# Performance work log

Measured on AMD Instinct MI355X. Metric: run time of the kernel, lower is better.

The kernel has to match this reference:

```python
import jax, jax.numpy as jnp
import numpy as np

DIM = 1024
N_HEADS = 16
HEAD_DIM = DIM // N_HEADS
SCALE = HEAD_DIM ** -0.5


def setup_inputs() -> dict:
    key = jax.random.key(0)
    ks = jax.random.split(key, 5)
    B, N = 2, 2048
    x = jax.random.normal(ks[0], (B, N, DIM), dtype=jnp.float32)
    # torch Linear: y = x @ W.T + b, W shape (out, in)
    qkv_w = jax.random.normal(ks[1], (3 * DIM, DIM), dtype=jnp.float32) * (DIM ** -0.5)
    qkv_b = jax.random.normal(ks[2], (3 * DIM,), dtype=jnp.float32) * 0.02
    proj_w = jax.random.normal(ks[3], (DIM, DIM), dtype=jnp.float32) * (DIM ** -0.5)
    proj_b = jax.random.normal(ks[4], (DIM,), dtype=jnp.float32) * 0.02
    return {"x": x, "qkv_w": qkv_w, "qkv_b": qkv_b, "proj_w": proj_w, "proj_b": proj_b}


def reference(x, qkv_w, qkv_b, proj_w, proj_b):
    B, N, D = x.shape
    qkv = x @ qkv_w.T + qkv_b                      # [B, N, 3D]
    qkv = qkv.reshape(B, N, 3, N_HEADS, HEAD_DIM)
    qkv = jnp.transpose(qkv, (2, 0, 3, 1, 4))      # [3, B, H, N, hd]
    q, k, v = qkv[0], qkv[1], qkv[2]
    dp = jnp.einsum('bhqd,bhkd->bhqk', q, k) * SCALE  # [B, H, N, N]
    attn = jax.nn.softmax(dp, axis=-1)
    wa = jnp.einsum('bhqk,bhkd->bhqd', attn, v)    # [B, H, N, hd]
    wa = jnp.transpose(wa, (0, 2, 1, 3)).reshape(B, N, D)
    return wa @ proj_w.T + proj_b
```

## Files before the change

### kernel.cpp

```cpp
#include <hip/hip_runtime.h>

#define BATCH 2
#define SEQ   2048
#define DIM   1024
#define NHEAD 16
#define HD    64
#define BH    (BATCH * NHEAD)
#define SCALE 0.125f
#define LOG2E 1.44269504f
#define NTK   16

typedef __attribute__((ext_vector_type(8))) short short8;
typedef __attribute__((ext_vector_type(4))) float f32x4;
typedef __attribute__((ext_vector_type(16))) float f32x16;
typedef __attribute__((ext_vector_type(2))) unsigned int uint2v;

#define MFMA16(a, b, c) __builtin_amdgcn_mfma_f32_16x16x32_bf16(a, b, c, 0, 0, 0)
#define MFMA32(a, b, c) __builtin_amdgcn_mfma_f32_32x32x16_bf16(a, b, c, 0, 0, 0)

__device__ __forceinline__ ushort f2bf(float f) {
    union { float f; unsigned u; } v;
    v.f = f;
    unsigned r = (v.u + 0x7FFF + ((v.u >> 16) & 1)) >> 16;
    return (ushort)r;
}

__device__ __forceinline__ uint4 ld8f_bf16(const float* p) {
    float4 f0 = *(const float4*)p;
    float4 f1 = *(const float4*)(p + 4);
    union { ushort us[8]; uint4 v; } u;
    u.us[0] = f2bf(f0.x); u.us[1] = f2bf(f0.y);
    u.us[2] = f2bf(f0.z); u.us[3] = f2bf(f0.w);
    u.us[4] = f2bf(f1.x); u.us[5] = f2bf(f1.y);
    u.us[6] = f2bf(f1.z); u.us[7] = f2bf(f1.w);
    return u.v;
}

__device__ __forceinline__ void gl_lds16(const ushort* g, ushort* l) {
    __builtin_amdgcn_global_load_lds(
        (const __attribute__((address_space(1))) unsigned int*)g,
        (__attribute__((address_space(3))) unsigned int*)l,
        16, 0, 0);
}

#define N_X  (BATCH * SEQ * DIM)
#define N_QW (3 * DIM * DIM)
#define N_PW (DIM * DIM)

__global__ __launch_bounds__(256) void cvt_kernel(
    const float* __restrict__ x, const float* __restrict__ qw,
    const float* __restrict__ pw, ushort* __restrict__ xb,
    ushort* __restrict__ qwb, ushort* __restrict__ pwb)
{
    const int i = (blockIdx.x * 256 + threadIdx.x) * 8;
    if (i < N_X)  *(uint4*)(xb  + i) = ld8f_bf16(x  + i);
    if (i < N_QW) *(uint4*)(qwb + i) = ld8f_bf16(qw + i);
    if (i < N_PW) *(uint4*)(pwb + i) = ld8f_bf16(pw + i);
}

template <int MODE, int WM, typename TOUT>
__global__ __launch_bounds__(256, 2) void gemm_bt(
    const ushort* __restrict__ A, const ushort* __restrict__ W,
    const float* __restrict__ bias, TOUT* __restrict__ out,
    int M, int Nout, int K)
{
    constexpr int BM = 2 * WM * 16;
    __shared__ __align__(16) ushort As[2][BM * 32];
    __shared__ __align__(16) ushort Bs[2][128 * 32];

    const int tid  = threadIdx.x;
    const int wave = tid >> 6, lane = tid & 63;
    const int quad = lane >> 4, l16 = lane & 15;
    const int wm = wave >> 1, wn = wave & 1;
    const int m0 = blockIdx.y * BM, n0 = blockIdx.x * 128;

    const int c0 = tid, c1 = tid + 256;
    const ushort* gA0 = A + (size_t)(m0 + (c0 >> 2)) * K + (c0 & 3) * 8;
    const ushort* gA1 = A + (size_t)(m0 + (c1 >> 2)) * K + (c1 & 3) * 8;
    const ushort* gB0 = W + (size_t)(n0 + (c0 >> 2)) * K + (c0 & 3) * 8;
    const ushort* gB1 = W + (size_t)(n0 + (c1 >> 2)) * K + (c1 & 3) * 8;

#define STAGE_G(buf, k0)                                                  \
    {                                                                     \
        gl_lds16(gA0 + (k0), &As[buf][(wave * 64) * 8]);                  \
        if (WM == 4) gl_lds16(gA1 + (k0), &As[buf][(wave * 64 + 256) * 8]); \
        gl_lds16(gB0 + (k0), &Bs[buf][(wave * 64) * 8]);                  \
        gl_lds16(gB1 + (k0), &Bs[buf][(wave * 64 + 256) * 8]);            \
    }

    f32x4 acc[WM][4];
#pragma unroll
    for (int i = 0; i < WM; i++)
#pragma unroll
        for (int j = 0; j < 4; j++) acc[i][j] = (f32x4){0.f, 0.f, 0.f, 0.f};

    const int KT = K >> 5;
    STAGE_G(0, 0)

    for (int kt = 0; kt < KT; kt++) {
        const int cur = kt & 1;
        __syncthreads();
        if (kt + 1 < KT) STAGE_G(cur ^ 1, (kt + 1) * 32)

        short8 af[WM], bfr[4];
#pragma unroll
        for (int mt = 0; mt < WM; mt++)
            af[mt] = *(const short8*)&As[cur][(wm * (WM * 16) + mt * 16 + l16) * 32 + quad * 8];
#pragma unroll
        for (int nt = 0; nt < 4; nt++)
            bfr[nt] = *(const short8*)&Bs[cur][(wn * 64 + nt * 16 + l16) * 32 + quad * 8];
#pragma unroll
        for (int mt = 0; mt < WM; mt++)
#pragma unroll
            for (int nt = 0; nt < 4; nt++)
                acc[mt][nt] = MFMA16(af[mt], bfr[nt], acc[mt][nt]);
    }

#pragma unroll
    for (int nt = 0; nt < 4; nt++) {
        const int n = n0 + wn * 64 + nt * 16 + l16;
        const float bv = bias[n];
#pragma unroll
        for (int mt = 0; mt < WM; mt++) {
            const int mBase = m0 + wm * (WM * 16) + mt * 16 + quad * 4;
#pragma unroll
            for (int r = 0; r < 4; r++) {
                const int m = mBase + r;
                float v = acc[mt][nt][r] + bv;
                if (MODE == 0) {
                    const int which = n >> 10, rem = n & 1023;
                    const int h = rem >> 6, d = rem & 63;
                    const int b = m >> 11, nq = m & 2047;
                    const int bh = b * NHEAD + h;
                    if (which == 0) v *= (SCALE * LOG2E);
                    size_t idx;
                    if (which == 2)
                        idx = (size_t)2 * BH * SEQ * HD + ((size_t)bh * HD + d) * SEQ + nq;
                    else
                        idx = (size_t)which * BH * SEQ * HD + ((size_t)bh * SEQ + nq) * HD + d;
                    ((ushort*)out)[idx] = f2bf(v);
                } else {
                    ((float*)out)[(size_t)m * Nout + n] = v;
                }
            }
        }
    }
#undef STAGE_G
}

__global__ __launch_bounds__(512, 4) void attn_kernel(
    const ushort* __restrict__ qkv, ushort* __restrict__ wa)
{
    __shared__ __align__(16) ushort Ks[2][2][64 * 64];
    __shared__ __align__(16) ushort Vs[2][2][64 * 64];

    const int tid  = threadIdx.x;
    const int wave = tid >> 6, lane = tid & 63;
    const int l31  = lane & 31, hb = lane >> 5;
    const int h2 = wave >> 2, w4 = wave & 3;

    const int l = blockIdx.x;
    const int bh = (l & 7) + 8 * (l >> 7);
    const int qi = (l >> 3) & 15;
    const int b = bh >> 4, head = bh & 15;

    const size_t hOff = (size_t)bh * SEQ * HD;
    const ushort* Q  = qkv + hOff;
    const ushort* Kg = qkv + (size_t)BH * SEQ * HD + hOff;
    const ushort* Vt = qkv + (size_t)2 * BH * SEQ * HD + hOff;
    const int q0 = qi * 128 + w4 * 32;

    short8 qf[4];
#pragma unroll
    for (int i = 0; i < 4; i++)
        qf[i] = *(const short8*)&Q[(size_t)(q0 + l31) * HD + i * 16 + hb * 8];

    f32x16 o0, o1;
#pragma unroll
    for (int r = 0; r < 16; r++) { o0[r] = 0.f; o1[r] = 0.f; }
    f32x4 lacc = (f32x4){0.f, 0.f, 0.f, 0.f};

    const int rr = lane >> 3;
    const int cc = ((lane & 7) ^ rr) * 8;
    const ushort* KgL = Kg + rr * HD + cc;
    const ushort* VtL = Vt + (size_t)rr * SEQ + cc;

#define STAGE(buf, kt)                                                          \
    {                                                                           \
        const size_t kO = (size_t)h2 * 1024 + (size_t)(kt) * 64;                \
        gl_lds16(KgL + (kO + w4 * 16    ) * HD, &Ks[h2][buf][(w4 * 16    ) * 64]); \
        gl_lds16(KgL + (kO + w4 * 16 + 8) * HD, &Ks[h2][buf][(w4 * 16 + 8) * 64]); \
        gl_lds16(VtL + (size_t)(w4 * 16    ) * SEQ + kO, &Vs[h2][buf][(w4 * 16    ) * 64]); \
        gl_lds16(VtL + (size_t)(w4 * 16 + 8) * SEQ + kO, &Vs[h2][buf][(w4 * 16 + 8) * 64]); \
    }

    STAGE(0, 0)

    const int swz = l31 & 7;

    for (int kt = 0; kt < NTK; kt++) {
        const int cur = kt & 1;
        __syncthreads();
        if (kt + 1 < NTK) STAGE(cur ^ 1, kt + 1)

        const ushort* kb_ = &Ks[h2][cur][0];
        const ushort* vb_ = &Vs[h2][cur][0];

        f32x16 z0, z1;
#pragma unroll
        for (int r = 0; r < 16; r++) { z0[r] = 0.f; z1[r] = 0.f; }

        __builtin_amdgcn_s_setprio(1);
#pragma unroll
        for (int i = 0; i < 4; i++) {
            short8 ka0 = *(const short8*)&kb_[(l31     ) * 64 + (((2*i + hb) ^ swz) * 8)];
            short8 ka1 = *(const short8*)&kb_[(32 + l31) * 64 + (((2*i + hb) ^ swz) * 8)];
            z0 = MFMA32(ka0, qf[i], z0);
            z1 = MFMA32(ka1, qf[i], z1);
        }
        __builtin_amdgcn_s_setprio(0);

        unsigned u[2][8];
#pragma unroll
        for (int r = 0; r < 16; r++) {
            const float p0 = __builtin_amdgcn_exp2f(z0[r]);
            const float p1 = __builtin_amdgcn_exp2f(z1[r]);
            z0[r] = p0; z1[r] = p1;
            lacc[r & 3] += p0 + p1;
        }
#pragma unroll
        for (int m = 0; m < 8; m++) {
            unsigned pk;
            asm("v_cvt_pk_bf16_f32 %0, %1, %2"
                : "=v"(pk) : "v"(z0[2*m]), "v"(z0[2*m + 1]));
            u[0][m] = pk;
            asm("v_cvt_pk_bf16_f32 %0, %1, %2"
                : "=v"(pk) : "v"(z1[2*m]), "v"(z1[2*m + 1]));
            u[1][m] = pk;
        }

        __builtin_amdgcn_s_setprio(1);
#pragma unroll
        for (int i = 0; i < 4; i++) {
            const int kb = i >> 1, ii = i & 1;
            uint2v s0 = __builtin_amdgcn_permlane32_swap(
                u[kb][4*ii + 0], u[kb][4*ii + 2], false, false);
            uint2v s1 = __builtin_amdgcn_permlane32_swap(
                u[kb][4*ii + 1], u[kb][4*ii + 3], false, false);
            union { unsigned w[4]; short8 s; } pf;
            pf.w[0] = s0[0]; pf.w[1] = s1[0]; pf.w[2] = s0[1]; pf.w[3] = s1[1];
            short8 vb0 = *(const short8*)&vb_[(l31     ) * 64 + (((2*i + hb) ^ swz) * 8)];
            short8 vb1 = *(const short8*)&vb_[(32 + l31) * 64 + (((2*i + hb) ^ swz) * 8)];
            o0 = MFMA32(pf.s, vb0, o0);
            o1 = MFMA32(pf.s, vb1, o1);
        }
        __builtin_amdgcn_s_setprio(0);
    }

    __syncthreads();

    float* Osc = (float*)&Ks[0][0][0];
    float* Lsc = (float*)&Vs[0][0][0];

    float lsum = lacc[0] + lacc[1] + lacc[2] + lacc[3];
    lsum += __shfl_xor(lsum, 32);
    if (lane < 32) Lsc[wave * 32 + l31] = lsum;

    if (h2 == 1) {
#pragma unroll
        for (int r = 0; r < 16; r++) {
            const int qr = (r & 3) + 8 * (r >> 2) + 4 * hb;
            Osc[w4 * 2048 + qr * 64 + l31]      = o0[r];
            Osc[w4 * 2048 + qr * 64 + 32 + l31] = o1[r];
        }
    }
    __syncthreads();

    if (h2 == 0) {
        const float inv = 1.f / (Lsc[w4 * 32 + l31] + Lsc[(4 + w4) * 32 + l31]);
#pragma unroll
        for (int r = 0; r < 16; r++) {
            const int qr = (r & 3) + 8 * (r >> 2) + 4 * hb;
            const float iv = __shfl(inv, qr);
            const float v0 = o0[r] + Osc[w4 * 2048 + qr * 64 + l31];
            const float v1 = o1[r] + Osc[w4 * 2048 + qr * 64 + 32 + l31];
            ushort* dst = wa + ((size_t)(b * SEQ + q0 + qr)) * DIM + head * HD + l31;
            dst[0]  = f2bf(v0 * iv);
            dst[32] = f2bf(v1 * iv);
        }
    }
#undef STAGE
}

extern "C" void kernel_launch(void* const* d_in, const int* in_sizes, int n_in,
                              void* d_out, int out_size, void* d_ws, size_t ws_size,
                              hipStream_t stream)
{
    const float* x      = (const float*)d_in[0];
    const float* qkv_w  = (const float*)d_in[1];
    const float* qkv_b  = (const float*)d_in[2];
    const float* proj_w = (const float*)d_in[3];
    const float* proj_b = (const float*)d_in[4];
    float* out = (float*)d_out;

    ushort* xb  = (ushort*)d_ws;
    ushort* qwb = xb  + (size_t)N_X;
    ushort* pwb = qwb + (size_t)N_QW;
    ushort* qkv = pwb + (size_t)N_PW;
    ushort* wa  = qkv + (size_t)3 * BH * SEQ * HD;

    const int M = BATCH * SEQ;
    dim3 blk(256);

    cvt_kernel<<<dim3((N_X / 8 + 255) / 256), blk, 0, stream>>>(
        x, qkv_w, proj_w, xb, qwb, pwb);

    gemm_bt<0, 4, ushort><<<dim3((3 * DIM) / 128, M / 128), blk, 0, stream>>>(
        xb, qwb, qkv_b, qkv, M, 3 * DIM, DIM);

    attn_kernel<<<dim3(512), dim3(512), 0, stream>>>(qkv, wa);

    gemm_bt<1, 2, float><<<dim3(DIM / 128, M / 64), blk, 0, stream>>>(
        wa, pwb, proj_b, out, M, DIM, DIM);
}
```

Baseline: 186.7 us.

## Give each attention wave 64 query rows to reuse K/V LDS fragments

```diff
diff --git a/kernel.cpp b/kernel.cpp
--- a/kernel.cpp
+++ b/kernel.cpp
@@ -148,7 +148,7 @@
 #undef STAGE_G
 }
 
-__global__ __launch_bounds__(512, 4) void attn_kernel(
+__global__ __launch_bounds__(256, 2) void attn_kernel(
     const ushort* __restrict__ qkv, ushort* __restrict__ wa)
 {
     __shared__ __align__(16) ushort Ks[2][2][64 * 64];
@@ -157,7 +157,7 @@
     const int tid  = threadIdx.x;
     const int wave = tid >> 6, lane = tid & 63;
     const int l31  = lane & 31, hb = lane >> 5;
-    const int h2 = wave >> 2, w4 = wave & 3;
+    const int h2 = wave >> 1, wq = wave & 1;
 
     const int l = blockIdx.x;
     const int bh = (l & 7) + 8 * (l >> 7);
@@ -168,17 +168,20 @@
     const ushort* Q  = qkv + hOff;
     const ushort* Kg = qkv + (size_t)BH * SEQ * HD + hOff;
     const ushort* Vt = qkv + (size_t)2 * BH * SEQ * HD + hOff;
-    const int q0 = qi * 128 + w4 * 32;
-
-    short8 qf[4];
-#pragma unroll
-    for (int i = 0; i < 4; i++)
-        qf[i] = *(const short8*)&Q[(size_t)(q0 + l31) * HD + i * 16 + hb * 8];
-
-    f32x16 o0, o1;
-#pragma unroll
-    for (int r = 0; r < 16; r++) { o0[r] = 0.f; o1[r] = 0.f; }
-    f32x4 lacc = (f32x4){0.f, 0.f, 0.f, 0.f};
+    const int q0 = qi * 128 + wq * 64;
+
+    short8 qf0[4], qf1[4];
+#pragma unroll
+    for (int i = 0; i < 4; i++) {
+        qf0[i] = *(const short8*)&Q[(size_t)(q0      + l31) * HD + i * 16 + hb * 8];
+        qf1[i] = *(const short8*)&Q[(size_t)(q0 + 32 + l31) * HD + i * 16 + hb * 8];
+    }
+
+    f32x16 o00, o01, o10, o11;
+#pragma unroll
+    for (int r = 0; r < 16; r++) { o00[r] = 0.f; o01[r] = 0.f; o10[r] = 0.f; o11[r] = 0.f; }
+    f32x4 lacc0 = (f32x4){0.f, 0.f, 0.f, 0.f};
+    f32x4 lacc1 = (f32x4){0.f, 0.f, 0.f, 0.f};
 
     const int rr = lane >> 3;
     const int cc = ((lane & 7) ^ rr) * 8;
@@ -188,10 +191,14 @@
 #define STAGE(buf, kt)                                                          \
     {                                                                           \
         const size_t kO = (size_t)h2 * 1024 + (size_t)(kt) * 64;                \
-        gl_lds16(KgL + (kO + w4 * 16    ) * HD, &Ks[h2][buf][(w4 * 16    ) * 64]); \
-        gl_lds16(KgL + (kO + w4 * 16 + 8) * HD, &Ks[h2][buf][(w4 * 16 + 8) * 64]); \
-        gl_lds16(VtL + (size_t)(w4 * 16    ) * SEQ + kO, &Vs[h2][buf][(w4 * 16    ) * 64]); \
-        gl_lds16(VtL + (size_t)(w4 * 16 + 8) * SEQ + kO, &Vs[h2][buf][(w4 * 16 + 8) * 64]); \
+        gl_lds16(KgL + (kO + wq * 32     ) * HD, &Ks[h2][buf][(wq * 32     ) * 64]); \
+        gl_lds16(KgL + (kO + wq * 32 +  8) * HD, &Ks[h2][buf][(wq * 32 +  8) * 64]); \
+        gl_lds16(KgL + (kO + wq * 32 + 16) * HD, &Ks[h2][buf][(wq * 32 + 16) * 64]); \
+        gl_lds16(KgL + (kO + wq * 32 + 24) * HD, &Ks[h2][buf][(wq * 32 + 24) * 64]); \
+        gl_lds16(VtL + (size_t)(wq * 32     ) * SEQ + kO, &Vs[h2][buf][(wq * 32     ) * 64]); \
+        gl_lds16(VtL + (size_t)(wq * 32 +  8) * SEQ + kO, &Vs[h2][buf][(wq * 32 +  8) * 64]); \
+        gl_lds16(VtL + (size_t)(wq * 32 + 16) * SEQ + kO, &Vs[h2][buf][(wq * 32 + 16) * 64]); \
+        gl_lds16(VtL + (size_t)(wq * 32 + 24) * SEQ + kO, &Vs[h2][buf][(wq * 32 + 24) * 64]); \
     }
 
     STAGE(0, 0)
@@ -206,37 +213,45 @@
         const ushort* kb_ = &Ks[h2][cur][0];
         const ushort* vb_ = &Vs[h2][cur][0];
 
-        f32x16 z0, z1;
-#pragma unroll
-        for (int r = 0; r < 16; r++) { z0[r] = 0.f; z1[r] = 0.f; }
+        f32x16 z00, z01, z10, z11;
+#pragma unroll
+        for (int r = 0; r < 16; r++) { z00[r] = 0.f; z01[r] = 0.f; z10[r] = 0.f; z11[r] = 0.f; }
 
         __builtin_amdgcn_s_setprio(1);
 #pragma unroll
         for (int i = 0; i < 4; i++) {
             short8 ka0 = *(const short8*)&kb_[(l31     ) * 64 + (((2*i + hb) ^ swz) * 8)];
             short8 ka1 = *(const short8*)&kb_[(32 + l31) * 64 + (((2*i + hb) ^ swz) * 8)];
-            z0 = MFMA32(ka0, qf[i], z0);
-            z1 = MFMA32(ka1, qf[i], z1);
+            z00 = MFMA32(ka0, qf0[i], z00);
+            z01 = MFMA32(ka1, qf0[i], z01);
+            z10 = MFMA32(ka0, qf1[i], z10);
+            z11 = MFMA32(ka1, qf1[i], z11);
         }
         __builtin_amdgcn_s_setprio(0);
 
-        unsigned u[2][8];
+        unsigned u0[2][8], u1[2][8];
 #pragma unroll
         for (int r = 0; r < 16; r++) {
-            const float p0 = __builtin_amdgcn_exp2f(z0[r]);
-            const float p1 = __builtin_amdgcn_exp2f(z1[r]);
-            z0[r] = p0; z1[r] = p1;
-            lacc[r & 3] += p0 + p1;
+            const float a0 = __builtin_amdgcn_exp2f(z00[r]);
+            const float a1 = __builtin_amdgcn_exp2f(z01[r]);
+            z00[r] = a0; z01[r] = a1;
+            lacc0[r & 3] += a0 + a1;
+            const float b0 = __builtin_amdgcn_exp2f(z10[r]);
+            const float b1 = __builtin_amdgcn_exp2f(z11[r]);
+            z10[r] = b0; z11[r] = b1;
+            lacc1[r & 3] += b0 + b1;
         }
 #pragma unroll
         for (int m = 0; m < 8; m++) {
             unsigned pk;
-            asm("v_cvt_pk_bf16_f32 %0, %1, %2"
-                : "=v"(pk) : "v"(z0[2*m]), "v"(z0[2*m + 1]));
-            u[0][m] = pk;
-            asm("v_cvt_pk_bf16_f32 %0, %1, %2"
-                : "=v"(pk) : "v"(z1[2*m]), "v"(z1[2*m + 1]));
-            u[1][m] = pk;
+            asm("v_cvt_pk_bf16_f32 %0, %1, %2" : "=v"(pk) : "v"(z00[2*m]), "v"(z00[2*m+1]));
+            u0[0][m] = pk;
+            asm("v_cvt_pk_bf16_f32 %0, %1, %2" : "=v"(pk) : "v"(z01[2*m]), "v"(z01[2*m+1]));
+            u0[1][m] = pk;
+            asm("v_cvt_pk_bf16_f32 %0, %1, %2" : "=v"(pk) : "v"(z10[2*m]), "v"(z10[2*m+1]));
+            u1[0][m] = pk;
+            asm("v_cvt_pk_bf16_f32 %0, %1, %2" : "=v"(pk) : "v"(z11[2*m]), "v"(z11[2*m+1]));
+            u1[1][m] = pk;
         }
 
         __builtin_amdgcn_s_setprio(1);
@@ -244,15 +259,24 @@
         for (int i = 0; i < 4; i++) {
             const int kb = i >> 1, ii = i & 1;
             uint2v s0 = __builtin_amdgcn_permlane32_swap(
-                u[kb][4*ii + 0], u[kb][4*ii + 2], false, false);
+                u0[kb][4*ii + 0], u0[kb][4*ii + 2], false, false);
             uint2v s1 = __builtin_amdgcn_permlane32_swap(
-                u[kb][4*ii + 1], u[kb][4*ii + 3], false, false);
-            union { unsigned w[4]; short8 s; } pf;
-            pf.w[0] = s0[0]; pf.w[1] = s1[0]; pf.w[2] = s0[1]; pf.w[3] = s1[1];
+                u0[kb][4*ii + 1], u0[kb][4*ii + 3], false, false);
+            union { unsigned w[4]; short8 s; } pf0;
+            pf0.w[0] = s0[0]; pf0.w[1] = s1[0]; pf0.w[2] = s0[1]; pf0.w[3] = s1[1];
+            uint2v t0 = __builtin_amdgcn_permlane32_swap(
+                u1[kb][4*ii + 0], u1[kb][4*ii + 2], false, false);
+            uint2v t1 = __builtin_amdgcn_permlane32_swap(
+                u1[kb][4*ii + 1], u1[kb][4*ii + 3], false, false);
+            union { unsigned w[4]; short8 s; } pf1;
+            pf1.w[0] = t0[0]; pf1.w[1] = t1[0]; pf1.w[2] = t0[1]; pf1.w[3] = t1[1];
+
             short8 vb0 = *(const short8*)&vb_[(l31     ) * 64 + (((2*i + hb) ^ swz) * 8)];
             short8 vb1 = *(const short8*)&vb_[(32 + l31) * 64 + (((2*i + hb) ^ swz) * 8)];
-            o0 = MFMA32(pf.s, vb0, o0);
-            o1 = MFMA32(pf.s, vb1, o1);
+            o00 = MFMA32(pf0.s, vb0, o00);
+            o01 = MFMA32(pf0.s, vb1, o01);
+            o10 = MFMA32(pf1.s, vb0, o10);
+            o11 = MFMA32(pf1.s, vb1, o11);
         }
         __builtin_amdgcn_s_setprio(0);
     }
@@ -262,31 +286,47 @@
     float* Osc = (float*)&Ks[0][0][0];
     float* Lsc = (float*)&Vs[0][0][0];
 
-    float lsum = lacc[0] + lacc[1] + lacc[2] + lacc[3];
-    lsum += __shfl_xor(lsum, 32);
-    if (lane < 32) Lsc[wave * 32 + l31] = lsum;
+    float ls0 = lacc0[0] + lacc0[1] + lacc0[2] + lacc0[3];
+    float ls1 = lacc1[0] + lacc1[1] + lacc1[2] + lacc1[3];
+    ls0 += __shfl_xor(ls0, 32);
+    ls1 += __shfl_xor(ls1, 32);
+    if (lane < 32) {
+        Lsc[((h2 * 2 + wq) * 2 + 0) * 32 + l31] = ls0;
+        Lsc[((h2 * 2 + wq) * 2 + 1) * 32 + l31] = ls1;
+    }
 
     if (h2 == 1) {
 #pragma unroll
         for (int r = 0; r < 16; r++) {
             const int qr = (r & 3) + 8 * (r >> 2) + 4 * hb;
-            Osc[w4 * 2048 + qr * 64 + l31]      = o0[r];
-            Osc[w4 * 2048 + qr * 64 + 32 + l31] = o1[r];
+            Osc[(wq * 64 + qr) * 64 + l31]           = o00[r];
+            Osc[(wq * 64 + qr) * 64 + 32 + l31]      = o01[r];
+            Osc[(wq * 64 + 32 + qr) * 64 + l31]      = o10[r];
+            Osc[(wq * 64 + 32 + qr) * 64 + 32 + l31] = o11[r];
         }
     }
     __syncthreads();
 
     if (h2 == 0) {
-        const float inv = 1.f / (Lsc[w4 * 32 + l31] + Lsc[(4 + w4) * 32 + l31]);
+        const float inv0 = 1.f / (Lsc[((0 * 2 + wq) * 2 + 0) * 32 + l31] +
+                                  Lsc[((1 * 2 + wq) * 2 + 0) * 32 + l31]);
+        const float inv1 = 1.f / (Lsc[((0 * 2 + wq) * 2 + 1) * 32 + l31] +
+                                  Lsc[((1 * 2 + wq) * 2 + 1) * 32 + l31]);
 #pragma unroll
         for (int r = 0; r < 16; r++) {
             const int qr = (r & 3) + 8 * (r >> 2) + 4 * hb;
-            const float iv = __shfl(inv, qr);
-            const float v0 = o0[r] + Osc[w4 * 2048 + qr * 64 + l31];
-            const float v1 = o1[r] + Osc[w4 * 2048 + qr * 64 + 32 + l31];
-            ushort* dst = wa + ((size_t)(b * SEQ + q0 + qr)) * DIM + head * HD + l31;
-            dst[0]  = f2bf(v0 * iv);
-            dst[32] = f2bf(v1 * iv);
+            const float iv0 = __shfl(inv0, qr);
+            const float iv1 = __shfl(inv1, qr);
+            const float v00 = o00[r] + Osc[(wq * 64 + qr) * 64 + l31];
+            const float v01 = o01[r] + Osc[(wq * 64 + qr) * 64 + 32 + l31];
+            const float v10 = o10[r] + Osc[(wq * 64 + 32 + qr) * 64 + l31];
+            const float v11 = o11[r] + Osc[(wq * 64 + 32 + qr) * 64 + 32 + l31];
+            ushort* dst0 = wa + ((size_t)(b * SEQ + q0 + qr)) * DIM + head * HD + l31;
+            ushort* dst1 = wa + ((size_t)(b * SEQ + q0 + 32 + qr)) * DIM + head * HD + l31;
+            dst0[0]  = f2bf(v00 * iv0);
+            dst0[32] = f2bf(v01 * iv0);
+            dst1[0]  = f2bf(v10 * iv1);
+            dst1[32] = f2bf(v11 * iv1);
         }
     }
 #undef STAGE
@@ -318,7 +358,7 @@
     gemm_bt<0, 4, ushort><<<dim3((3 * DIM) / 128, M / 128), blk, 0, stream>>>(
         xb, qwb, qkv_b, qkv, M, 3 * DIM, DIM);
 
-    attn_kernel<<<dim3(512), dim3(512), 0, stream>>>(qkv, wa);
+    attn_kernel<<<dim3(512), dim3(256), 0, stream>>>(qkv, wa);
 
     gemm_bt<1, 2, float><<<dim3(DIM / 128, M / 64), blk, 0, stream>>>(
         wa, pwb, proj_b, out, M, DIM, DIM);
```

Measured after the change: 190.2 us. About the same (+1.8%).

## Software-pipeline attention loop so PV of previous tile overlaps current QK and exp

Applied to the files above, without the earlier changes.

```diff
diff --git a/kernel.cpp b/kernel.cpp
--- a/kernel.cpp
+++ b/kernel.cpp
@@ -148,7 +148,7 @@
 #undef STAGE_G
 }
 
-__global__ __launch_bounds__(512, 4) void attn_kernel(
+__global__ __launch_bounds__(512, 2) void attn_kernel(
     const ushort* __restrict__ qkv, ushort* __restrict__ wa)
 {
     __shared__ __align__(16) ushort Ks[2][2][64 * 64];
@@ -198,64 +198,95 @@
 
     const int swz = l31 & 7;
 
-    for (int kt = 0; kt < NTK; kt++) {
-        const int cur = kt & 1;
-        __syncthreads();
-        if (kt + 1 < NTK) STAGE(cur ^ 1, kt + 1)
-
-        const ushort* kb_ = &Ks[h2][cur][0];
-        const ushort* vb_ = &Vs[h2][cur][0];
-
-        f32x16 z0, z1;
-#pragma unroll
-        for (int r = 0; r < 16; r++) { z0[r] = 0.f; z1[r] = 0.f; }
-
-        __builtin_amdgcn_s_setprio(1);
-#pragma unroll
-        for (int i = 0; i < 4; i++) {
-            short8 ka0 = *(const short8*)&kb_[(l31     ) * 64 + (((2*i + hb) ^ swz) * 8)];
-            short8 ka1 = *(const short8*)&kb_[(32 + l31) * 64 + (((2*i + hb) ^ swz) * 8)];
-            z0 = MFMA32(ka0, qf[i], z0);
-            z1 = MFMA32(ka1, qf[i], z1);
-        }
-        __builtin_amdgcn_s_setprio(0);
-
-        unsigned u[2][8];
-#pragma unroll
-        for (int r = 0; r < 16; r++) {
-            const float p0 = __builtin_amdgcn_exp2f(z0[r]);
-            const float p1 = __builtin_amdgcn_exp2f(z1[r]);
-            z0[r] = p0; z1[r] = p1;
-            lacc[r & 3] += p0 + p1;
-        }
-#pragma unroll
-        for (int m = 0; m < 8; m++) {
-            unsigned pk;
-            asm("v_cvt_pk_bf16_f32 %0, %1, %2"
-                : "=v"(pk) : "v"(z0[2*m]), "v"(z0[2*m + 1]));
-            u[0][m] = pk;
-            asm("v_cvt_pk_bf16_f32 %0, %1, %2"
-                : "=v"(pk) : "v"(z1[2*m]), "v"(z1[2*m + 1]));
-            u[1][m] = pk;
-        }
-
-        __builtin_amdgcn_s_setprio(1);
-#pragma unroll
-        for (int i = 0; i < 4; i++) {
-            const int kb = i >> 1, ii = i & 1;
-            uint2v s0 = __builtin_amdgcn_permlane32_swap(
-                u[kb][4*ii + 0], u[kb][4*ii + 2], false, false);
-            uint2v s1 = __builtin_amdgcn_permlane32_swap(
-                u[kb][4*ii + 1], u[kb][4*ii + 3], false, false);
-            union { unsigned w[4]; short8 s; } pf;
-            pf.w[0] = s0[0]; pf.w[1] = s1[0]; pf.w[2] = s0[1]; pf.w[3] = s1[1];
-            short8 vb0 = *(const short8*)&vb_[(l31     ) * 64 + (((2*i + hb) ^ swz) * 8)];
-            short8 vb1 = *(const short8*)&vb_[(32 + l31) * 64 + (((2*i + hb) ^ swz) * 8)];
-            o0 = MFMA32(pf.s, vb0, o0);
-            o1 = MFMA32(pf.s, vb1, o1);
-        }
-        __builtin_amdgcn_s_setprio(0);
-    }
+    unsigned uA[2][8], uB[2][8];
+    short8 vA[4][2], vB[4][2];
+#pragma unroll
+    for (int kb = 0; kb < 2; kb++)
+#pragma unroll
+        for (int m = 0; m < 8; m++) uA[kb][m] = 0u;
+#pragma unroll
+    for (int i = 0; i < 4; i++) {
+        vA[i][0] = (short8){0,0,0,0,0,0,0,0};
+        vA[i][1] = (short8){0,0,0,0,0,0,0,0};
+    }
+
+#define QKPV_ITER(kt, cur, UP, VP, UN, VN)                                      \
+    {                                                                           \
+        __syncthreads();                             \
+        if ((kt) + 1 < NTK) STAGE((cur) ^ 1, (kt) + 1)                          \
+        const ushort* kb_ = &Ks[h2][cur][0];                                    \
+        const ushort* vb_ = &Vs[h2][cur][0];                                    \
+        f32x16 z0, z1;                                                          \
+        _Pragma("unroll")                                                       \
+        for (int r = 0; r < 16; r++) { z0[r] = 0.f; z1[r] = 0.f; }              \
+        __builtin_amdgcn_s_setprio(1);                                          \
+        _Pragma("unroll")                                                       \
+        for (int i = 0; i < 4; i++) {                                           \
+            short8 ka0 = *(const short8*)&kb_[(l31     ) * 64 + (((2*i + hb) ^ swz) * 8)]; \
+            short8 ka1 = *(const short8*)&kb_[(32 + l31) * 64 + (((2*i + hb) ^ swz) * 8)]; \
+            z0 = MFMA32(ka0, qf[i], z0);                                        \
+            z1 = MFMA32(ka1, qf[i], z1);                                        \
+        }                                                                       \
+        __builtin_amdgcn_s_setprio(0);                                          \
+        _Pragma("unroll")                                                       \
+        for (int i = 0; i < 4; i++) {                                           \
+            VN[i][0] = *(const short8*)&vb_[(l31     ) * 64 + (((2*i + hb) ^ swz) * 8)]; \
+            VN[i][1] = *(const short8*)&vb_[(32 + l31) * 64 + (((2*i + hb) ^ swz) * 8)]; \
+        }                                                                       \
+            \
+        __builtin_amdgcn_s_setprio(1);                                          \
+        _Pragma("unroll")                                                       \
+        for (int i = 0; i < 4; i++) {                                           \
+            const int kb = i >> 1, ii = i & 1;                                  \
+            uint2v s0 = __builtin_amdgcn_permlane32_swap(                       \
+                UP[kb][4*ii + 0], UP[kb][4*ii + 2], false, false);              \
+            uint2v s1 = __builtin_amdgcn_permlane32_swap(                       \
+                UP[kb][4*ii + 1], UP[kb][4*ii + 3], false, false);              \
+            union { unsigned w[4]; short8 s; } pf;                              \
+            pf.w[0] = s0[0]; pf.w[1] = s1[0]; pf.w[2] = s0[1]; pf.w[3] = s1[1]; \
+            o0 = MFMA32(pf.s, VP[i][0], o0);                                    \
+            o1 = MFMA32(pf.s, VP[i][1], o1);                                    \
+        }                                                                       \
+        __builtin_amdgcn_s_setprio(0);                                          \
+              \
+        _Pragma("unroll")                                                       \
+        for (int r = 0; r < 16; r++) {                                          \
+            const float p0 = __builtin_amdgcn_exp2f(z0[r]);                     \
+            const float p1 = __builtin_amdgcn_exp2f(z1[r]);                     \
+            z0[r] = p0; z1[r] = p1;                                             \
+            lacc[r & 3] += p0 + p1;                                             \
+        }                                                                       \
+        _Pragma("unroll")                                                       \
+        for (int m = 0; m < 8; m++) {                                           \
+            unsigned pk;                                                        \
+            asm("v_cvt_pk_bf16_f32 %0, %1, %2"                                  \
+                : "=v"(pk) : "v"(z0[2*m]), "v"(z0[2*m + 1]));                   \
+            UN[0][m] = pk;                                                      \
+            asm("v_cvt_pk_bf16_f32 %0, %1, %2"                                  \
+                : "=v"(pk) : "v"(z1[2*m]), "v"(z1[2*m + 1]));                   \
+            UN[1][m] = pk;                                                      \
+        }                                                                       \
+    }
+
+    for (int kt = 0; kt < NTK; kt += 2) {
+        QKPV_ITER(kt,     0, uA, vA, uB, vB)
+        QKPV_ITER(kt + 1, 1, uB, vB, uA, vA)
+    }
+
+    __builtin_amdgcn_s_setprio(1);
+#pragma unroll
+    for (int i = 0; i < 4; i++) {
+        const int kb = i >> 1, ii = i & 1;
+        uint2v s0 = __builtin_amdgcn_permlane32_swap(
+            uA[kb][4*ii + 0], uA[kb][4*ii + 2], false, false);
+        uint2v s1 = __builtin_amdgcn_permlane32_swap(
+            uA[kb][4*ii + 1], uA[kb][4*ii + 3], false, false);
+        union { unsigned w[4]; short8 s; } pf;
+        pf.w[0] = s0[0]; pf.w[1] = s1[0]; pf.w[2] = s0[1]; pf.w[3] = s1[1];
+        o0 = MFMA32(pf.s, vA[i][0], o0);
+        o1 = MFMA32(pf.s, vA[i][1], o1);
+    }
+    __builtin_amdgcn_s_setprio(0);
 
     __syncthreads();
 
@@ -290,6 +321,7 @@
         }
     }
 #undef STAGE
+#undef QKPV_ITER
 }
 
 extern "C" void kernel_launch(void* const* d_in, const int* in_sizes, int n_in,
```

Result: no change. 189.0 us (+1.2%).

## Change K/V shared-memory swizzle to paired 8-byte halves with matching global layout

Applied to the files above, without the earlier changes.

```diff
diff --git a/kernel.cpp b/kernel.cpp
--- a/kernel.cpp
+++ b/kernel.cpp
@@ -11,6 +11,7 @@
 #define NTK   16
 
 typedef __attribute__((ext_vector_type(8))) short short8;
+typedef __attribute__((ext_vector_type(4))) short short4v;
 typedef __attribute__((ext_vector_type(4))) float f32x4;
 typedef __attribute__((ext_vector_type(16))) float f32x16;
 typedef __attribute__((ext_vector_type(2))) unsigned int uint2v;
@@ -41,6 +42,13 @@
         (const __attribute__((address_space(1))) unsigned int*)g,
         (__attribute__((address_space(3))) unsigned int*)l,
         16, 0, 0);
+}
+
+__device__ __forceinline__ short8 ld_op(const ushort* base, int a1) {
+    union { short4v h[2]; short8 v; } u;
+    u.h[0] = *(const short4v*)&base[a1];
+    u.h[1] = *(const short4v*)&base[a1 ^ 4];
+    return u.v;
 }
 
 #define N_X  (BATCH * SEQ * DIM)
@@ -134,10 +142,13 @@
                     const int bh = b * NHEAD + h;
                     if (which == 0) v *= (SCALE * LOG2E);
                     size_t idx;
-                    if (which == 2)
-                        idx = (size_t)2 * BH * SEQ * HD + ((size_t)bh * HD + d) * SEQ + nq;
-                    else
-                        idx = (size_t)which * BH * SEQ * HD + ((size_t)bh * SEQ + nq) * HD + d;
+                    if (which == 2) {
+                        const int nqs = (d & 1) ? (nq ^ 4) : nq;
+                        idx = (size_t)2 * BH * SEQ * HD + ((size_t)bh * HD + d) * SEQ + nqs;
+                    } else {
+                        const int ds = (which == 1 && (nq & 1)) ? (d ^ 4) : d;
+                        idx = (size_t)which * BH * SEQ * HD + ((size_t)bh * SEQ + nq) * HD + ds;
+                    }
                     ((ushort*)out)[idx] = f2bf(v);
                 } else {
                     ((float*)out)[(size_t)m * Nout + n] = v;
@@ -181,22 +192,25 @@
     f32x4 lacc = (f32x4){0.f, 0.f, 0.f, 0.f};
 
     const int rr = lane >> 3;
-    const int cc = ((lane & 7) ^ rr) * 8;
-    const ushort* KgL = Kg + rr * HD + cc;
-    const ushort* VtL = Vt + (size_t)rr * SEQ + cc;
+    const int cA = (((lane & 7) ^ (rr >> 1)) & 7) * 8;
+    const ushort* KgA = Kg + rr * HD + cA;
+    const ushort* KgB = Kg + rr * HD + (cA ^ 32);
+    const ushort* VtA = Vt + (size_t)rr * SEQ + cA;
+    const ushort* VtB = Vt + (size_t)rr * SEQ + (cA ^ 32);
 
 #define STAGE(buf, kt)                                                          \
     {                                                                           \
         const size_t kO = (size_t)h2 * 1024 + (size_t)(kt) * 64;                \
-        gl_lds16(KgL + (kO + w4 * 16    ) * HD, &Ks[h2][buf][(w4 * 16    ) * 64]); \
-        gl_lds16(KgL + (kO + w4 * 16 + 8) * HD, &Ks[h2][buf][(w4 * 16 + 8) * 64]); \
-        gl_lds16(VtL + (size_t)(w4 * 16    ) * SEQ + kO, &Vs[h2][buf][(w4 * 16    ) * 64]); \
-        gl_lds16(VtL + (size_t)(w4 * 16 + 8) * SEQ + kO, &Vs[h2][buf][(w4 * 16 + 8) * 64]); \
+        gl_lds16(KgA + (kO + w4 * 16    ) * HD, &Ks[h2][buf][(w4 * 16    ) * 64]); \
+        gl_lds16(KgB + (kO + w4 * 16 + 8) * HD, &Ks[h2][buf][(w4 * 16 + 8) * 64]); \
+        gl_lds16(VtA + (size_t)(w4 * 16    ) * SEQ + kO, &Vs[h2][buf][(w4 * 16    ) * 64]); \
+        gl_lds16(VtB + (size_t)(w4 * 16 + 8) * SEQ + kO, &Vs[h2][buf][(w4 * 16 + 8) * 64]); \
     }
 
     STAGE(0, 0)
 
-    const int swz = l31 & 7;
+    const int sw2 = (l31 >> 1) & 7;
+    const int pb  = (l31 & 1) * 4;
 
     for (int kt = 0; kt < NTK; kt++) {
         const int cur = kt & 1;
@@ -213,8 +227,9 @@
         __builtin_amdgcn_s_setprio(1);
 #pragma unroll
         for (int i = 0; i < 4; i++) {
-            short8 ka0 = *(const short8*)&kb_[(l31     ) * 64 + (((2*i + hb) ^ swz) * 8)];
-            short8 ka1 = *(const short8*)&kb_[(32 + l31) * 64 + (((2*i + hb) ^ swz) * 8)];
+            const int co = (((2 * i + hb) ^ sw2) * 8) + pb;
+            short8 ka0 = ld_op(kb_, (l31     ) * 64 + co);
+            short8 ka1 = ld_op(kb_, (32 + l31) * 64 + co);
             z0 = MFMA32(ka0, qf[i], z0);
             z1 = MFMA32(ka1, qf[i], z1);
         }
@@ -249,8 +264,9 @@
                 u[kb][4*ii + 1], u[kb][4*ii + 3], false, false);
             union { unsigned w[4]; short8 s; } pf;
             pf.w[0] = s0[0]; pf.w[1] = s1[0]; pf.w[2] = s0[1]; pf.w[3] = s1[1];
-            short8 vb0 = *(const short8*)&vb_[(l31     ) * 64 + (((2*i + hb) ^ swz) * 8)];
-            short8 vb1 = *(const short8*)&vb_[(32 + l31) * 64 + (((2*i + hb) ^ swz) * 8)];
+            const int co = (((2 * i + hb) ^ sw2) * 8) + pb;
+            short8 vb0 = ld_op(vb_, (l31     ) * 64 + co);
+            short8 vb1 = ld_op(vb_, (32 + l31) * 64 + co);
             o0 = MFMA32(pf.s, vb0, o0);
             o1 = MFMA32(pf.s, vb1, o1);
         }
```

After: 192.3 us. +3.0%, slower.
